# Kernel tuning notes

Hardware: AMD Instinct MI355X
Metric: run time of the kernel (lower is better)

Reference implementation:

```python
import jax, jax.numpy as jnp
import numpy as np
import math

B, H, LQ, LK, D = 2, 16, 2048, 2048, 128

def setup_inputs() -> dict:
    key = jax.random.key(0)
    kq, kk, kv, km = jax.random.split(key, 4)
    return {
        "query": jax.random.normal(kq, (B, H, LQ, D), dtype=jnp.float32),
        "key": jax.random.normal(kk, (B, H, LK, D), dtype=jnp.float32),
        "value": jax.random.normal(kv, (B, H, LK, D), dtype=jnp.float32),
        # positive integer multiplicities in [1, 8] so log() is finite
        "key_multiplicities": jax.random.randint(km, (B, LK), 1, 9, dtype=jnp.int32),
    }

def reference(query, key, value, key_multiplicities):
    scale = 1.0 / math.sqrt(query.shape[-1])
    # scores: [B, H, Lq, Lk]
    scores = jnp.einsum("bhqd,bhkd->bhqk", query, key) * scale
    # additive log-multiplicity bias, broadcast over heads and queries
    log_mult = jnp.log(key_multiplicities.astype(scores.dtype))  # [B, Lk]
    scores = scores + log_mult[:, None, None, :]
    attn = jax.nn.softmax(scores, axis=-1)
    # dropout_p = 0.0 -> identity
    return jnp.einsum("bhqk,bhkd->bhqd", attn, value)
```

## Files before the change

kernel.cpp:

```cpp
#include <hip/hip_runtime.h>
#include <hip/hip_bf16.h>

constexpr int B_  = 2;
constexpr int H_  = 16;
constexpr int LQ_ = 2048;
constexpr int LK_ = 2048;
constexpr int D_  = 128;

constexpr int BM = 128;
constexpr int BN = 64;
constexpr int NT = LK_ / BN;
constexpr int TILE_SH = 64 * 128;

constexpr float SCALE_LOG2E = 0.12751649734586414f;
constexpr float M_STATIC = 16.0f;

typedef short s16x8 __attribute__((ext_vector_type(8)));
typedef float f32x16 __attribute__((ext_vector_type(16)));

#define MFMA32 __builtin_amdgcn_mfma_f32_32x32x16_bf16

#if __has_builtin(__builtin_amdgcn_exp2f)
#define EXP2(x) __builtin_amdgcn_exp2f(x)
#else
#define EXP2(x) exp2f(x)
#endif
#if __has_builtin(__builtin_amdgcn_logf)
#define LOG2(x) __builtin_amdgcn_logf(x)
#else
#define LOG2(x) log2f(x)
#endif

static __device__ __forceinline__ int pk2bf(float a, float b) {
  float2 t{a, b};
  __hip_bfloat162 h = __float22bfloat162_rn(t);
  return *reinterpret_cast<int*>(&h);
}

static __device__ __forceinline__ void dma16(const short* g, short* l) {
  __builtin_amdgcn_global_load_lds(
      (const __attribute__((address_space(1))) void*)g,
      (__attribute__((address_space(3))) void*)l, 16, 0, 0);
}

__global__ __launch_bounds__(256)
void prep(const float* __restrict__ kg, const float* __restrict__ vg,
          const int* __restrict__ multg, short* __restrict__ wsK,
          short* __restrict__ wsV, float* __restrict__ wsBias) {
  __shared__ float tileF[64 * 133];
  const int tid = threadIdx.x;
  const int wg  = blockIdx.x;
  const float* kp = kg + (size_t)wg * 64 * 128;
  const float* vp = vg + (size_t)wg * 64 * 128;
  short* wk = wsK + (size_t)wg * TILE_SH;
  short* wv = wsV + (size_t)wg * TILE_SH;

#pragma unroll
  for (int i = 0; i < 4; ++i) {
    int idx = tid + i * 256;
    int row = idx >> 4, blk = idx & 15;
    const float* src = kp + row * 128 + blk * 8;
    float4 a = *(const float4*)src;
    float4 c4 = *(const float4*)(src + 4);
    int4 t;
    t.x = pk2bf(a.x, a.y);  t.y = pk2bf(a.z, a.w);
    t.z = pk2bf(c4.x, c4.y); t.w = pk2bf(c4.z, c4.w);
    int pos = blk ^ (row & 15);
    *(int4*)&wk[row * 128 + pos * 8] = t;
  }

#pragma unroll
  for (int i = 0; i < 8; ++i) {
    int idx = tid + i * 256;
    int key = idx >> 5, d0 = (idx & 31) * 4;
    float4 a = *(const float4*)(vp + key * 128 + d0);
    float* dst = &tileF[key * 133 + d0];
    dst[0] = a.x; dst[1] = a.y; dst[2] = a.z; dst[3] = a.w;
  }
  __syncthreads();
#pragma unroll
  for (int i = 0; i < 4; ++i) {
    int idx = tid + i * 256;
    int d = idx >> 3, kgrp = idx & 7;
    float v[8];
#pragma unroll
    for (int j = 0; j < 8; ++j) v[j] = tileF[(kgrp * 8 + j) * 133 + d];
    int4 t;
    t.x = pk2bf(v[0], v[1]); t.y = pk2bf(v[2], v[3]);
    t.z = pk2bf(v[4], v[5]); t.w = pk2bf(v[6], v[7]);
    int pos = kgrp ^ ((d >> 1) & 7);
    *(int4*)&wv[d * 64 + pos * 8] = t;
  }

  if (wg < 8) {
    int b = wg >> 2;
    for (int j = tid; j < 512; j += 256) {
      int i0 = (wg & 3) * 512 + j;
      wsBias[b * LK_ + i0] = LOG2((float)multg[b * LK_ + i0]) - M_STATIC;
    }
  }
}

__global__ __launch_bounds__(256, 2)
void attn_fwd(const float* __restrict__ qg, const short* __restrict__ wsK,
              const short* __restrict__ wsV, const float* __restrict__ wsBias,
              float* __restrict__ outg) {
  __shared__ alignas(16) short Kbuf[2][TILE_SH];
  __shared__ alignas(16) short Vbuf[2][TILE_SH];
  __shared__ alignas(16) float biasLds[LK_];

  const int tid  = threadIdx.x;
  const int w    = tid >> 6;
  const int lane = tid & 63;
  const int lq   = lane & 31;
  const int hi   = lane >> 5;

  const int L   = blockIdx.y * gridDim.x + blockIdx.x;
  const int k8  = L >> 3;
  const int qb  = k8 & 15;
  const int bh  = (L & 7) * 4 + (k8 >> 4);
  const int b   = bh >> 4;

  const float* qptr = qg + (size_t)bh * LQ_ * D_;
  float*       optr = outg + (size_t)bh * LQ_ * D_;
  const short* kws  = wsK + (size_t)bh * NT * TILE_SH;
  const short* vws  = wsV + (size_t)bh * NT * TILE_SH;
  const float* bias = wsBias + b * LK_;

  const int q0 = qb * BM + w * 32;

  {
    int i = tid * 8;
    float4 a = *(const float4*)&bias[i];
    float4 c = *(const float4*)&bias[i + 4];
    *(float4*)&biasLds[i] = a;
    *(float4*)&biasLds[i + 4] = c;
  }

  s16x8 qf[8];
  {
    const float* qrow = qptr + (size_t)(q0 + lq) * D_ + hi * 8;
#pragma unroll
    for (int kf = 0; kf < 8; ++kf) {
      float4 a = *(const float4*)(qrow + kf * 16);
      float4 c = *(const float4*)(qrow + kf * 16 + 4);
      int4 t;
      t.x = pk2bf(a.x * SCALE_LOG2E, a.y * SCALE_LOG2E);
      t.y = pk2bf(a.z * SCALE_LOG2E, a.w * SCALE_LOG2E);
      t.z = pk2bf(c.x * SCALE_LOG2E, c.y * SCALE_LOG2E);
      t.w = pk2bf(c.z * SCALE_LOG2E, c.w * SCALE_LOG2E);
      qf[kf] = *(s16x8*)&t;
    }
  }

  int4 onesI{0x3F803F80, 0x3F803F80, 0x3F803F80, 0x3F803F80};
  const s16x8 onesf = *(const s16x8*)&onesI;

  f32x16 o[4], oL;
#pragma unroll
  for (int dt = 0; dt < 4; ++dt)
#pragma unroll
    for (int r = 0; r < 16; ++r) o[dt][r] = 0.f;
#pragma unroll
  for (int r = 0; r < 16; ++r) oL[r] = 0.f;

  auto dmaK = [&](int kt) {
    const short* gK = kws + (size_t)kt * TILE_SH;
    short* lb = &Kbuf[kt & 1][0];
#pragma unroll
    for (int i = 0; i < 4; ++i) {
      int off = (w * 4 + i) * 512;
      dma16(gK + off + lane * 8, lb + off);
    }
  };
  auto dmaV = [&](int kt) {
    const short* gV = vws + (size_t)kt * TILE_SH;
    short* lb = &Vbuf[kt & 1][0];
#pragma unroll
    for (int i = 0; i < 4; ++i) {
      int off = (w * 4 + i) * 512;
      dma16(gV + off + lane * 8, lb + off);
    }
  };

  auto qk = [&](int kt, f32x16* St) {
    const float* bl = &biasLds[kt * BN];
#pragma unroll
    for (int t = 0; t < 2; ++t)
#pragma unroll
      for (int g = 0; g < 4; ++g) {
        float4 bv = *(const float4*)&bl[t * 32 + g * 8 + hi * 4];
        St[t][g * 4 + 0] = bv.x; St[t][g * 4 + 1] = bv.y;
        St[t][g * 4 + 2] = bv.z; St[t][g * 4 + 3] = bv.w;
      }
    const short* kb0 = &Kbuf[kt & 1][0];
    __builtin_amdgcn_s_setprio(1);
#pragma unroll
    for (int t = 0; t < 2; ++t) {
      const short* kb = &kb0[(t * 32 + lq) * 128];
#pragma unroll
      for (int kf = 0; kf < 8; ++kf) {
        s16x8 kfr = *(const s16x8*)&kb[((2 * kf + hi) ^ (lq & 15)) * 8];
        St[t] = MFMA32(kfr, qf[kf], St[t], 0, 0, 0);
      }
    }
    __builtin_amdgcn_s_setprio(0);
  };

  auto body = [&](int t, f32x16* Sc, f32x16* Sn, bool doNext, bool doK) {
    __syncthreads();
    if (doNext) dmaV(t + 1);
    if (doK)    dmaK(t + 2);
    __builtin_amdgcn_sched_barrier(0);

    if (doNext) qk(t + 1, Sn);

#pragma unroll
    for (int tt = 0; tt < 2; ++tt)
#pragma unroll
      for (int r = 0; r < 16; ++r) Sc[tt][r] = EXP2(Sc[tt][r]);

    s16x8 pf[2][2];
#pragma unroll
    for (int tt = 0; tt < 2; ++tt) {
      int P[8];
#pragma unroll
      for (int i = 0; i < 8; ++i) P[i] = pk2bf(Sc[tt][2 * i], Sc[tt][2 * i + 1]);
#pragma unroll
      for (int ks = 0; ks < 2; ++ks) {
        int a0 = P[4 * ks + 0], a1 = P[4 * ks + 1];
        int b0 = P[4 * ks + 2], b1 = P[4 * ks + 3];
        asm("v_permlane32_swap_b32 %0, %1" : "+v"(a0), "+v"(b0));
        asm("v_permlane32_swap_b32 %0, %1" : "+v"(a1), "+v"(b1));
        int4 tt2{a0, a1, b0, b1};
        pf[tt][ks] = *(s16x8*)&tt2;
      }
    }

    const short* vb0 = &Vbuf[t & 1][0];
    __builtin_amdgcn_s_setprio(1);
#pragma unroll
    for (int tt = 0; tt < 2; ++tt)
#pragma unroll
      for (int ks = 0; ks < 2; ++ks)
        oL = MFMA32(pf[tt][ks], onesf, oL, 0, 0, 0);
#pragma unroll
    for (int dt = 0; dt < 4; ++dt) {
      const short* vb = &vb0[(dt * 32 + lq) * 64];
#pragma unroll
      for (int tt = 0; tt < 2; ++tt)
#pragma unroll
        for (int ks = 0; ks < 2; ++ks) {
          s16x8 vf = *(const s16x8*)
              &vb[((tt * 4 + ks * 2 + hi) ^ ((lq >> 1) & 7)) * 8];
          o[dt] = MFMA32(pf[tt][ks], vf, o[dt], 0, 0, 0);
        }
    }
    __builtin_amdgcn_s_setprio(0);
  };

  dmaK(0); dmaV(0);
  __syncthreads();
  dmaK(1);
  f32x16 StA[2], StB[2];
  qk(0, StA);

  for (int t = 0; t < NT - 2; t += 2) {
    body(t,     StA, StB, true, true);
    body(t + 1, StB, StA, true, true);
  }
  body(NT - 2, StA, StB, true,  false);
  body(NT - 1, StB, StA, false, false);

  float li[16];
#pragma unroll
  for (int r = 0; r < 16; ++r) li[r] = 1.0f / oL[r];
#pragma unroll
  for (int dt = 0; dt < 4; ++dt)
#pragma unroll
    for (int r = 0; r < 16; ++r) {
      int row = q0 + (r & 3) + 8 * (r >> 2) + 4 * hi;
      optr[(size_t)row * D_ + dt * 32 + lq] = o[dt][r] * li[r];
    }
}

extern "C" void kernel_launch(void* const* d_in, const int* in_sizes, int n_in,
                              void* d_out, int out_size, void* d_ws, size_t ws_size,
                              hipStream_t stream) {
  const float* q = (const float*)d_in[0];
  const float* k = (const float*)d_in[1];
  const float* v = (const float*)d_in[2];
  const int* mult = (const int*)d_in[3];
  float* out = (float*)d_out;

  constexpr size_t KV_BYTES = (size_t)B_ * H_ * LK_ * D_ * 2;
  short* wsK = (short*)d_ws;
  short* wsV = (short*)((char*)d_ws + KV_BYTES);
  float* wsBias = (float*)((char*)d_ws + 2 * KV_BYTES);

  prep<<<dim3(B_ * H_ * NT), dim3(256), 0, stream>>>(k, v, mult, wsK, wsV, wsBias);

  dim3 grid(LQ_ / BM, B_ * H_);
  attn_fwd<<<grid, dim3(256), 0, stream>>>(q, wsK, wsV, wsBias, out);
}
```

Before: 197.1 us.

## Split key range across two warp groups with LDS merge of partial outputs

The block grows from 256 to 512 threads. Two groups of four warps each process half of the key sequence in 32-key subtiles, and their partial outputs and row sums are merged through shared memory at the end. This is possible because the kernel uses a static max, so partial softmax sums add directly. The aim is more waves per CU for latency hiding, at the cost of smaller MFMA batches per step, a loss of the previous QK/PV software pipelining, extra synchronisation, and a merge epilogue.

```diff
diff --git a/kernel.cpp b/kernel.cpp
--- a/kernel.cpp
+++ b/kernel.cpp
@@ -8,9 +8,10 @@
 constexpr int D_  = 128;
 
 constexpr int BM = 128;
-constexpr int BN = 64;
-constexpr int NT = LK_ / BN;
+constexpr int BN = 32;
+constexpr int NSUB = 1024 / BN;
 constexpr int TILE_SH = 64 * 128;
+constexpr int SUB_SH  = 32 * 128;
 
 constexpr float SCALE_LOG2E = 0.12751649734586414f;
 constexpr float M_STATIC = 16.0f;
@@ -101,12 +102,11 @@
   }
 }
 
-__global__ __launch_bounds__(256, 2)
+__global__ __launch_bounds__(512, 4)
 void attn_fwd(const float* __restrict__ qg, const short* __restrict__ wsK,
               const short* __restrict__ wsV, const float* __restrict__ wsBias,
               float* __restrict__ outg) {
-  __shared__ alignas(16) short Kbuf[2][TILE_SH];
-  __shared__ alignas(16) short Vbuf[2][TILE_SH];
+  __shared__ alignas(16) short tiles[2][2][2 * SUB_SH];
   __shared__ alignas(16) float biasLds[LK_];
 
   const int tid  = threadIdx.x;
@@ -114,6 +114,8 @@
   const int lane = tid & 63;
   const int lq   = lane & 31;
   const int hi   = lane >> 5;
+  const int wq   = w & 3;
+  const int kgp  = w >> 2;
 
   const int L   = blockIdx.y * gridDim.x + blockIdx.x;
   const int k8  = L >> 3;
@@ -123,18 +125,15 @@
 
   const float* qptr = qg + (size_t)bh * LQ_ * D_;
   float*       optr = outg + (size_t)bh * LQ_ * D_;
-  const short* kws  = wsK + (size_t)bh * NT * TILE_SH;
-  const short* vws  = wsV + (size_t)bh * NT * TILE_SH;
+  const short* kws  = wsK + (size_t)bh * (LK_ / 64) * TILE_SH;
+  const short* vws  = wsV + (size_t)bh * (LK_ / 64) * TILE_SH;
   const float* bias = wsBias + b * LK_;
 
-  const int q0 = qb * BM + w * 32;
+  const int q0 = qb * BM + wq * 32;
 
   {
-    int i = tid * 8;
-    float4 a = *(const float4*)&bias[i];
-    float4 c = *(const float4*)&bias[i + 4];
-    *(float4*)&biasLds[i] = a;
-    *(float4*)&biasLds[i + 4] = c;
+    int i = tid * 4;
+    *(float4*)&biasLds[i] = *(const float4*)&bias[i];
   }
 
   s16x8 qf[8];
@@ -164,124 +163,159 @@
 #pragma unroll
   for (int r = 0; r < 16; ++r) oL[r] = 0.f;
 
-  auto dmaK = [&](int kt) {
-    const short* gK = kws + (size_t)kt * TILE_SH;
-    short* lb = &Kbuf[kt & 1][0];
-#pragma unroll
-    for (int i = 0; i < 4; ++i) {
-      int off = (w * 4 + i) * 512;
+  auto dmaKV = [&](int t) {
+    int u  = kgp * NSUB + t;
+    int Tk = u >> 1, s = u & 1;
+    short* lb = &tiles[kgp][t & 1][0];
+    const short* gK = kws + (size_t)Tk * TILE_SH + s * SUB_SH;
+    const short* gV = vws + (size_t)Tk * TILE_SH;
+#pragma unroll
+    for (int i = 0; i < 2; ++i) {
+      int off = (wq * 2 + i) * 512;
       dma16(gK + off + lane * 8, lb + off);
     }
+    short* lv = lb + SUB_SH;
+#pragma unroll
+    for (int i = 0; i < 2; ++i) {
+      int off = (wq * 2 + i) * 512;
+      int oo  = off + lane * 8;
+      int src = ((oo >> 5) << 6) + ((s ^ ((oo >> 8) & 1)) << 5) + (oo & 31);
+      dma16(gV + src, lv + off);
+    }
   };
-  auto dmaV = [&](int kt) {
-    const short* gV = vws + (size_t)kt * TILE_SH;
-    short* lb = &Vbuf[kt & 1][0];
-#pragma unroll
-    for (int i = 0; i < 4; ++i) {
-      int off = (w * 4 + i) * 512;
-      dma16(gV + off + lane * 8, lb + off);
-    }
-  };
-
-  auto qk = [&](int kt, f32x16* St) {
-    const float* bl = &biasLds[kt * BN];
-#pragma unroll
-    for (int t = 0; t < 2; ++t)
-#pragma unroll
-      for (int g = 0; g < 4; ++g) {
-        float4 bv = *(const float4*)&bl[t * 32 + g * 8 + hi * 4];
-        St[t][g * 4 + 0] = bv.x; St[t][g * 4 + 1] = bv.y;
-        St[t][g * 4 + 2] = bv.z; St[t][g * 4 + 3] = bv.w;
-      }
-    const short* kb0 = &Kbuf[kt & 1][0];
+
+  dmaKV(0);
+
+  for (int t = 0; t < NSUB; ++t) {
+    __syncthreads();
+    if (t + 1 < NSUB) dmaKV(t + 1);
+    __builtin_amdgcn_sched_barrier(0);
+
+    const short* kb0 = &tiles[kgp][t & 1][0];
+    const short* vb0 = kb0 + SUB_SH;
+    const int u = kgp * NSUB + t;
+
+    f32x16 St;
+    const float* bl = &biasLds[u * 32];
+#pragma unroll
+    for (int g = 0; g < 4; ++g) {
+      float4 bv = *(const float4*)&bl[g * 8 + hi * 4];
+      St[g * 4 + 0] = bv.x; St[g * 4 + 1] = bv.y;
+      St[g * 4 + 2] = bv.z; St[g * 4 + 3] = bv.w;
+    }
+
+    const short* kb = &kb0[lq * 128];
     __builtin_amdgcn_s_setprio(1);
 #pragma unroll
-    for (int t = 0; t < 2; ++t) {
-      const short* kb = &kb0[(t * 32 + lq) * 128];
-#pragma unroll
-      for (int kf = 0; kf < 8; ++kf) {
-        s16x8 kfr = *(const s16x8*)&kb[((2 * kf + hi) ^ (lq & 15)) * 8];
-        St[t] = MFMA32(kfr, qf[kf], St[t], 0, 0, 0);
-      }
+    for (int kf = 0; kf < 8; ++kf) {
+      s16x8 kfr = *(const s16x8*)&kb[((2 * kf + hi) ^ (lq & 15)) * 8];
+      St = MFMA32(kfr, qf[kf], St, 0, 0, 0);
     }
     __builtin_amdgcn_s_setprio(0);
-  };
-
-  auto body = [&](int t, f32x16* Sc, f32x16* Sn, bool doNext, bool doK) {
-    __syncthreads();
-    if (doNext) dmaV(t + 1);
-    if (doK)    dmaK(t + 2);
-    __builtin_amdgcn_sched_barrier(0);
-
-    if (doNext) qk(t + 1, Sn);
-
-#pragma unroll
-    for (int tt = 0; tt < 2; ++tt)
-#pragma unroll
-      for (int r = 0; r < 16; ++r) Sc[tt][r] = EXP2(Sc[tt][r]);
-
-    s16x8 pf[2][2];
-#pragma unroll
-    for (int tt = 0; tt < 2; ++tt) {
+
+#pragma unroll
+    for (int r = 0; r < 16; ++r) St[r] = EXP2(St[r]);
+
+    s16x8 pf[2];
+    {
       int P[8];
 #pragma unroll
-      for (int i = 0; i < 8; ++i) P[i] = pk2bf(Sc[tt][2 * i], Sc[tt][2 * i + 1]);
+      for (int i = 0; i < 8; ++i) P[i] = pk2bf(St[2 * i], St[2 * i + 1]);
 #pragma unroll
       for (int ks = 0; ks < 2; ++ks) {
         int a0 = P[4 * ks + 0], a1 = P[4 * ks + 1];
         int b0 = P[4 * ks + 2], b1 = P[4 * ks + 3];
         asm("v_permlane32_swap_b32 %0, %1" : "+v"(a0), "+v"(b0));
         asm("v_permlane32_swap_b32 %0, %1" : "+v"(a1), "+v"(b1));
-        int4 tt2{a0, a1, b0, b1};
-        pf[tt][ks] = *(s16x8*)&tt2;
-      }
-    }
-
-    const short* vb0 = &Vbuf[t & 1][0];
+        int4 tt{a0, a1, b0, b1};
+        pf[ks] = *(s16x8*)&tt;
+      }
+    }
+
     __builtin_amdgcn_s_setprio(1);
 #pragma unroll
-    for (int tt = 0; tt < 2; ++tt)
-#pragma unroll
-      for (int ks = 0; ks < 2; ++ks)
-        oL = MFMA32(pf[tt][ks], onesf, oL, 0, 0, 0);
+    for (int ks = 0; ks < 2; ++ks)
+      oL = MFMA32(pf[ks], onesf, oL, 0, 0, 0);
 #pragma unroll
     for (int dt = 0; dt < 4; ++dt) {
-      const short* vb = &vb0[(dt * 32 + lq) * 64];
-#pragma unroll
-      for (int tt = 0; tt < 2; ++tt)
-#pragma unroll
-        for (int ks = 0; ks < 2; ++ks) {
-          s16x8 vf = *(const s16x8*)
-              &vb[((tt * 4 + ks * 2 + hi) ^ ((lq >> 1) & 7)) * 8];
-          o[dt] = MFMA32(pf[tt][ks], vf, o[dt], 0, 0, 0);
-        }
+      int d = dt * 32 + lq;
+      const short* vb = &vb0[d * 32];
+#pragma unroll
+      for (int ks = 0; ks < 2; ++ks) {
+        s16x8 vf = *(const s16x8*)&vb[(((ks * 2 + hi) ^ ((d >> 1) & 3)) * 8)];
+        o[dt] = MFMA32(pf[ks], vf, o[dt], 0, 0, 0);
+      }
     }
     __builtin_amdgcn_s_setprio(0);
-  };
-
-  dmaK(0); dmaV(0);
-  __syncthreads();
-  dmaK(1);
-  f32x16 StA[2], StB[2];
-  qk(0, StA);
-
-  for (int t = 0; t < NT - 2; t += 2) {
-    body(t,     StA, StB, true, true);
-    body(t + 1, StB, StA, true, true);
-  }
-  body(NT - 2, StA, StB, true,  false);
-  body(NT - 1, StB, StA, false, false);
-
-  float li[16];
-#pragma unroll
-  for (int r = 0; r < 16; ++r) li[r] = 1.0f / oL[r];
-#pragma unroll
-  for (int dt = 0; dt < 4; ++dt)
-#pragma unroll
-    for (int r = 0; r < 16; ++r) {
-      int row = q0 + (r & 3) + 8 * (r >> 2) + 4 * hi;
-      optr[(size_t)row * D_ + dt * 32 + lq] = o[dt][r] * li[r];
-    }
+  }
+
+  float4* mrg = (float4*)&tiles[0][0][0];
+  __syncthreads();
+  if (kgp == 0) {
+#pragma unroll
+    for (int dt = 0; dt < 2; ++dt)
+#pragma unroll
+      for (int rq = 0; rq < 4; ++rq) {
+        float4 x{o[dt][rq * 4 + 0], o[dt][rq * 4 + 1],
+                 o[dt][rq * 4 + 2], o[dt][rq * 4 + 3]};
+        mrg[((wq * 2 + dt) * 4 + rq) * 64 + lane] = x;
+      }
+  }
+  __syncthreads();
+  if (kgp == 1) {
+#pragma unroll
+    for (int dt = 0; dt < 2; ++dt)
+#pragma unroll
+      for (int rq = 0; rq < 4; ++rq) {
+        float4 x = mrg[((wq * 2 + dt) * 4 + rq) * 64 + lane];
+        o[dt][rq * 4 + 0] += x.x; o[dt][rq * 4 + 1] += x.y;
+        o[dt][rq * 4 + 2] += x.z; o[dt][rq * 4 + 3] += x.w;
+      }
+  }
+  __syncthreads();
+  if (kgp == 0) {
+#pragma unroll
+    for (int dt = 0; dt < 2; ++dt)
+#pragma unroll
+      for (int rq = 0; rq < 4; ++rq) {
+        float4 x{o[dt + 2][rq * 4 + 0], o[dt + 2][rq * 4 + 1],
+                 o[dt + 2][rq * 4 + 2], o[dt + 2][rq * 4 + 3]};
+        mrg[((wq * 2 + dt) * 4 + rq) * 64 + lane] = x;
+      }
+#pragma unroll
+    for (int rq = 0; rq < 4; ++rq) {
+      float4 x{oL[rq * 4 + 0], oL[rq * 4 + 1], oL[rq * 4 + 2], oL[rq * 4 + 3]};
+      mrg[2048 + (wq * 4 + rq) * 64 + lane] = x;
+    }
+  }
+  __syncthreads();
+  if (kgp == 1) {
+#pragma unroll
+    for (int dt = 0; dt < 2; ++dt)
+#pragma unroll
+      for (int rq = 0; rq < 4; ++rq) {
+        float4 x = mrg[((wq * 2 + dt) * 4 + rq) * 64 + lane];
+        o[dt + 2][rq * 4 + 0] += x.x; o[dt + 2][rq * 4 + 1] += x.y;
+        o[dt + 2][rq * 4 + 2] += x.z; o[dt + 2][rq * 4 + 3] += x.w;
+      }
+#pragma unroll
+    for (int rq = 0; rq < 4; ++rq) {
+      float4 x = mrg[2048 + (wq * 4 + rq) * 64 + lane];
+      oL[rq * 4 + 0] += x.x; oL[rq * 4 + 1] += x.y;
+      oL[rq * 4 + 2] += x.z; oL[rq * 4 + 3] += x.w;
+    }
+
+    float li[16];
+#pragma unroll
+    for (int r = 0; r < 16; ++r) li[r] = 1.0f / oL[r];
+#pragma unroll
+    for (int dt = 0; dt < 4; ++dt)
+#pragma unroll
+      for (int r = 0; r < 16; ++r) {
+        int row = q0 + (r & 3) + 8 * (r >> 2) + 4 * hi;
+        optr[(size_t)row * D_ + dt * 32 + lq] = o[dt][r] * li[r];
+      }
+  }
 }
 
 extern "C" void kernel_launch(void* const* d_in, const int* in_sizes, int n_in,
@@ -298,8 +332,8 @@
   short* wsV = (short*)((char*)d_ws + KV_BYTES);
   float* wsBias = (float*)((char*)d_ws + 2 * KV_BYTES);
 
-  prep<<<dim3(B_ * H_ * NT), dim3(256), 0, stream>>>(k, v, mult, wsK, wsV, wsBias);
+  prep<<<dim3(B_ * H_ * (LK_ / 64)), dim3(256), 0, stream>>>(k, v, mult, wsK, wsV, wsBias);
 
   dim3 grid(LQ_ / BM, B_ * H_);
-  attn_fwd<<<grid, dim3(256), 0, stream>>>(q, wsK, wsV, wsBias, out);
-}
+  attn_fwd<<<grid, dim3(512), 0, stream>>>(q, wsK, wsV, wsBias, out);
+}
```

Measured after the change: 337.3 us. 71.1% more time.

## Switch to 32-key subtiles with register-staged triple-buffered K/V loads

Applied to the files above, without the earlier changes.

Replaces the direct global-to-LDS DMA double buffer of 64-key tiles with 32-key subtiles held in a three-slot LDS ring. Each subtile is loaded into registers after the PV MFMAs and written to LDS after the softmax of the next iteration. The V subtile is rearranged on the fly from the 64-wide prep layout with a remapped swizzle. The aim is deeper prefetch and smaller per-step working sets, in exchange for more barriers per key, extra VGPR staging, and LDS writes issued by the threads instead of DMA.

```diff
diff --git a/kernel.cpp b/kernel.cpp
--- a/kernel.cpp
+++ b/kernel.cpp
@@ -8,9 +8,10 @@
 constexpr int D_  = 128;
 
 constexpr int BM = 128;
-constexpr int BN = 64;
-constexpr int NT = LK_ / BN;
+constexpr int BN = 32;
+constexpr int NSUB = LK_ / BN;
 constexpr int TILE_SH = 64 * 128;
+constexpr int SUB_SH  = 32 * 128;
 
 constexpr float SCALE_LOG2E = 0.12751649734586414f;
 constexpr float M_STATIC = 16.0f;
@@ -35,12 +36,6 @@
   float2 t{a, b};
   __hip_bfloat162 h = __float22bfloat162_rn(t);
   return *reinterpret_cast<int*>(&h);
-}
-
-static __device__ __forceinline__ void dma16(const short* g, short* l) {
-  __builtin_amdgcn_global_load_lds(
-      (const __attribute__((address_space(1))) void*)g,
-      (__attribute__((address_space(3))) void*)l, 16, 0, 0);
 }
 
 __global__ __launch_bounds__(256)
@@ -105,8 +100,8 @@
 void attn_fwd(const float* __restrict__ qg, const short* __restrict__ wsK,
               const short* __restrict__ wsV, const float* __restrict__ wsBias,
               float* __restrict__ outg) {
-  __shared__ alignas(16) short Kbuf[2][TILE_SH];
-  __shared__ alignas(16) short Vbuf[2][TILE_SH];
+  __shared__ alignas(16) short KB[3][SUB_SH];
+  __shared__ alignas(16) short VB[3][SUB_SH];
   __shared__ alignas(16) float biasLds[LK_];
 
   const int tid  = threadIdx.x;
@@ -123,8 +118,8 @@
 
   const float* qptr = qg + (size_t)bh * LQ_ * D_;
   float*       optr = outg + (size_t)bh * LQ_ * D_;
-  const short* kws  = wsK + (size_t)bh * NT * TILE_SH;
-  const short* vws  = wsV + (size_t)bh * NT * TILE_SH;
+  const short* kws  = wsK + (size_t)bh * (LK_ / 64) * TILE_SH;
+  const short* vws  = wsV + (size_t)bh * (LK_ / 64) * TILE_SH;
   const float* bias = wsBias + b * LK_;
 
   const int q0 = qb * BM + w * 32;
@@ -164,113 +159,115 @@
 #pragma unroll
   for (int r = 0; r < 16; ++r) oL[r] = 0.f;
 
-  auto dmaK = [&](int kt) {
-    const short* gK = kws + (size_t)kt * TILE_SH;
-    short* lb = &Kbuf[kt & 1][0];
-#pragma unroll
-    for (int i = 0; i < 4; ++i) {
-      int off = (w * 4 + i) * 512;
-      dma16(gK + off + lane * 8, lb + off);
+  int4 stg[4];
+  auto loads = [&](int u) {
+    int Tk = u >> 1, s = u & 1;
+    const short* gK = kws + (size_t)Tk * TILE_SH + s * SUB_SH;
+    const short* gV = vws + (size_t)Tk * TILE_SH;
+#pragma unroll
+    for (int i = 0; i < 2; ++i) {
+      int off = w * 1024 + i * 512 + lane * 8;
+      stg[i] = *(const int4*)(gK + off);
+    }
+#pragma unroll
+    for (int i = 0; i < 2; ++i) {
+      int oo = w * 1024 + i * 512 + lane * 8;
+      int src = ((oo >> 5) << 6) + ((s ^ ((oo >> 8) & 1)) << 5) + (oo & 31);
+      stg[2 + i] = *(const int4*)(gV + src);
     }
   };
-  auto dmaV = [&](int kt) {
-    const short* gV = vws + (size_t)kt * TILE_SH;
-    short* lb = &Vbuf[kt & 1][0];
-#pragma unroll
-    for (int i = 0; i < 4; ++i) {
-      int off = (w * 4 + i) * 512;
-      dma16(gV + off + lane * 8, lb + off);
+  auto writes = [&](int sl) {
+#pragma unroll
+    for (int i = 0; i < 2; ++i) {
+      int off = w * 1024 + i * 512 + lane * 8;
+      *(int4*)&KB[sl][off] = stg[i];
+    }
+#pragma unroll
+    for (int i = 0; i < 2; ++i) {
+      int off = w * 1024 + i * 512 + lane * 8;
+      *(int4*)&VB[sl][off] = stg[2 + i];
     }
   };
 
-  auto qk = [&](int kt, f32x16* St) {
-    const float* bl = &biasLds[kt * BN];
-#pragma unroll
-    for (int t = 0; t < 2; ++t)
-#pragma unroll
-      for (int g = 0; g < 4; ++g) {
-        float4 bv = *(const float4*)&bl[t * 32 + g * 8 + hi * 4];
-        St[t][g * 4 + 0] = bv.x; St[t][g * 4 + 1] = bv.y;
-        St[t][g * 4 + 2] = bv.z; St[t][g * 4 + 3] = bv.w;
-      }
-    const short* kb0 = &Kbuf[kt & 1][0];
+  auto qk = [&](int u, int sl, f32x16& St) {
+    const float* bl = &biasLds[u * 32];
+#pragma unroll
+    for (int g = 0; g < 4; ++g) {
+      float4 bv = *(const float4*)&bl[g * 8 + hi * 4];
+      St[g * 4 + 0] = bv.x; St[g * 4 + 1] = bv.y;
+      St[g * 4 + 2] = bv.z; St[g * 4 + 3] = bv.w;
+    }
+    const short* kb = &KB[sl][lq * 128];
     __builtin_amdgcn_s_setprio(1);
 #pragma unroll
-    for (int t = 0; t < 2; ++t) {
-      const short* kb = &kb0[(t * 32 + lq) * 128];
-#pragma unroll
-      for (int kf = 0; kf < 8; ++kf) {
-        s16x8 kfr = *(const s16x8*)&kb[((2 * kf + hi) ^ (lq & 15)) * 8];
-        St[t] = MFMA32(kfr, qf[kf], St[t], 0, 0, 0);
-      }
+    for (int kf = 0; kf < 8; ++kf) {
+      s16x8 kfr = *(const s16x8*)&kb[((2 * kf + hi) ^ (lq & 15)) * 8];
+      St = MFMA32(kfr, qf[kf], St, 0, 0, 0);
     }
     __builtin_amdgcn_s_setprio(0);
   };
 
-  auto body = [&](int t, f32x16* Sc, f32x16* Sn, bool doNext, bool doK) {
-    __syncthreads();
-    if (doNext) dmaV(t + 1);
-    if (doK)    dmaK(t + 2);
-    __builtin_amdgcn_sched_barrier(0);
-
-    if (doNext) qk(t + 1, Sn);
-
-#pragma unroll
-    for (int tt = 0; tt < 2; ++tt)
-#pragma unroll
-      for (int r = 0; r < 16; ++r) Sc[tt][r] = EXP2(Sc[tt][r]);
-
-    s16x8 pf[2][2];
-#pragma unroll
-    for (int tt = 0; tt < 2; ++tt) {
+  auto body = [&](int t, f32x16& Sc, f32x16& Sn, bool dn, bool dw, bool dl) {
+    if (dn) qk(t + 1, (t + 1) % 3, Sn);
+
+#pragma unroll
+    for (int r = 0; r < 16; ++r) Sc[r] = EXP2(Sc[r]);
+
+    s16x8 pf[2];
+    {
       int P[8];
 #pragma unroll
-      for (int i = 0; i < 8; ++i) P[i] = pk2bf(Sc[tt][2 * i], Sc[tt][2 * i + 1]);
+      for (int i = 0; i < 8; ++i) P[i] = pk2bf(Sc[2 * i], Sc[2 * i + 1]);
 #pragma unroll
       for (int ks = 0; ks < 2; ++ks) {
         int a0 = P[4 * ks + 0], a1 = P[4 * ks + 1];
         int b0 = P[4 * ks + 2], b1 = P[4 * ks + 3];
         asm("v_permlane32_swap_b32 %0, %1" : "+v"(a0), "+v"(b0));
         asm("v_permlane32_swap_b32 %0, %1" : "+v"(a1), "+v"(b1));
-        int4 tt2{a0, a1, b0, b1};
-        pf[tt][ks] = *(s16x8*)&tt2;
+        int4 tt{a0, a1, b0, b1};
+        pf[ks] = *(s16x8*)&tt;
       }
     }
 
-    const short* vb0 = &Vbuf[t & 1][0];
+    if (dw) writes((t + 2) % 3);
+
+    const short* vb0 = &VB[t % 3][0];
     __builtin_amdgcn_s_setprio(1);
 #pragma unroll
-    for (int tt = 0; tt < 2; ++tt)
-#pragma unroll
-      for (int ks = 0; ks < 2; ++ks)
-        oL = MFMA32(pf[tt][ks], onesf, oL, 0, 0, 0);
+    for (int ks = 0; ks < 2; ++ks)
+      oL = MFMA32(pf[ks], onesf, oL, 0, 0, 0);
 #pragma unroll
     for (int dt = 0; dt < 4; ++dt) {
-      const short* vb = &vb0[(dt * 32 + lq) * 64];
-#pragma unroll
-      for (int tt = 0; tt < 2; ++tt)
-#pragma unroll
-        for (int ks = 0; ks < 2; ++ks) {
-          s16x8 vf = *(const s16x8*)
-              &vb[((tt * 4 + ks * 2 + hi) ^ ((lq >> 1) & 7)) * 8];
-          o[dt] = MFMA32(pf[tt][ks], vf, o[dt], 0, 0, 0);
-        }
+      int d = dt * 32 + lq;
+      const short* vb = &vb0[d * 32];
+#pragma unroll
+      for (int ks = 0; ks < 2; ++ks) {
+        s16x8 vf = *(const s16x8*)&vb[(((ks * 2 + hi) ^ ((d >> 1) & 3)) * 8)];
+        o[dt] = MFMA32(pf[ks], vf, o[dt], 0, 0, 0);
+      }
     }
     __builtin_amdgcn_s_setprio(0);
+
+    if (dl) loads(t + 3);
+
+    __syncthreads();
   };
 
-  dmaK(0); dmaV(0);
+  loads(0); writes(0);
+  loads(1); writes(1);
+  loads(2);
   __syncthreads();
-  dmaK(1);
-  f32x16 StA[2], StB[2];
-  qk(0, StA);
-
-  for (int t = 0; t < NT - 2; t += 2) {
-    body(t,     StA, StB, true, true);
-    body(t + 1, StB, StA, true, true);
-  }
-  body(NT - 2, StA, StB, true,  false);
-  body(NT - 1, StB, StA, false, false);
+  f32x16 StA, StB;
+  qk(0, 0, StA);
+
+  for (int t = 0; t < NSUB - 4; t += 2) {
+    body(t,     StA, StB, true, true, true);
+    body(t + 1, StB, StA, true, true, true);
+  }
+  body(NSUB - 4, StA, StB, true,  true,  true);
+  body(NSUB - 3, StB, StA, true,  true,  false);
+  body(NSUB - 2, StA, StB, true,  false, false);
+  body(NSUB - 1, StB, StA, false, false, false);
 
   float li[16];
 #pragma unroll
@@ -298,7 +295,7 @@
   short* wsV = (short*)((char*)d_ws + KV_BYTES);
   float* wsBias = (float*)((char*)d_ws + 2 * KV_BYTES);
 
-  prep<<<dim3(B_ * H_ * NT), dim3(256), 0, stream>>>(k, v, mult, wsK, wsV, wsBias);
+  prep<<<dim3(B_ * H_ * (LK_ / 64)), dim3(256), 0, stream>>>(k, v, mult, wsK, wsV, wsBias);
 
   dim3 grid(LQ_ / BM, B_ * H_);
   attn_fwd<<<grid, dim3(256), 0, stream>>>(q, wsK, wsV, wsBias, out);
```

New measurement: 243.0 us. +23.3%, slower.
